# Kernel optimization log

Hardware: AMD Instinct MI355X
Metric: run time of the kernel (lower is better)

## Reference

```python
import jax, jax.numpy as jnp
import numpy as np

B, S, D = 4, 4096, 1024          # batch, seq, in/out features
H = 128                          # controller_hidden_dim
K = 8                            # num_spectral_bases
R = 8                            # low_rank_rank
OR = 8                           # orthogonal_rank
RES_SCALE = 1.0; SPEC_SCALE = 1.0; LR_SCALE = 1.0; ROT_SCALE = 1.0
LN_EPS = 1e-5


def setup_inputs() -> dict:
    key = jax.random.key(0)
    ks = jax.random.split(key, 16)
    g = lambda k, shape, scale=0.02: jax.random.normal(k, shape, jnp.float32) * scale
    return dict(
        x=jax.random.normal(ks[0], (B, S, D), jnp.float32),
        # base linear (teacher-aligned base)
        W_base=g(ks[1], (D, D)), b_base=jnp.zeros((D,), jnp.float32),
        # pooled-token conditioner: LayerNorm -> Linear -> GELU -> Linear
        ln_g=jnp.ones((D,), jnp.float32), ln_b=jnp.zeros((D,), jnp.float32),
        Wc1=g(ks[2], (D, H)), bc1=jnp.zeros((H,), jnp.float32),
        Wc2=g(ks[3], (H, H)), bc2=jnp.zeros((H,), jnp.float32),
        # gate heads
        W_rot_gate=g(ks[4], (H, 1)), b_rot_gate=jnp.zeros((1,), jnp.float32),
        W_rot_coeff=g(ks[5], (H, OR)), b_rot_coeff=jnp.zeros((OR,), jnp.float32),
        W_spec_gate=g(ks[6], (H, K)), b_spec_gate=jnp.zeros((K,), jnp.float32),
        W_lr_coeff=g(ks[7], (H, R)), b_lr_coeff=jnp.zeros((R,), jnp.float32),
        # spectral basis operator: input basis U, output basis V
        U_spec=g(ks[8], (K, D), 0.05), V_spec=g(ks[9], (K, D), 0.05),
        # low-rank residual operator
        U_lr=g(ks[10], (R, D), 0.05), V_lr=g(ks[11], (R, D), 0.05),
        # low-rank orthogonal mixer generators (skew-symmetric pairs)
        A_orth=g(ks[12], (OR, D), 0.05), B_orth=g(ks[13], (OR, D), 0.05),
    )


def reference(x, W_base, b_base, ln_g, ln_b, Wc1, bc1, Wc2, bc2,
              W_rot_gate, b_rot_gate, W_rot_coeff, b_rot_coeff,
              W_spec_gate, b_spec_gate, W_lr_coeff, b_lr_coeff,
              U_spec, V_spec, U_lr, V_lr, A_orth, B_orth):
    # --- pooled token conditioner: mean pool -> LN -> MLP -> hidden h [B,H]
    pooled = x.mean(axis=1)                                   # [B, D]
    mu = pooled.mean(-1, keepdims=True)
    var = pooled.var(-1, keepdims=True)
    z = (pooled - mu) * jax.lax.rsqrt(var + LN_EPS) * ln_g + ln_b
    h = jax.nn.gelu(z @ Wc1 + bc1) @ Wc2 + bc2                # [B, H]

    # --- conditioner-produced gates
    rot_gate = jax.nn.sigmoid(h @ W_rot_gate + b_rot_gate)    # [B, 1]
    rot_coeff = jnp.tanh(h @ W_rot_coeff + b_rot_coeff)       # [B, OR]
    spec_gate = jnp.tanh(h @ W_spec_gate + b_spec_gate)       # [B, K]
    lr_coeff = jnp.tanh(h @ W_lr_coeff + b_lr_coeff)          # [B, R]

    # --- low-rank orthogonal mixer: x_rot = x + gate * x @ G^T,
    #     G = sum_k c_k (a_k b_k^T - b_k a_k^T) (skew-symmetric generator)
    pa = jnp.einsum('bsi,ki->bsk', x, A_orth)
    pb = jnp.einsum('bsi,ki->bsk', x, B_orth)
    rot = (jnp.einsum('bsk,bk,ki->bsi', pb, rot_coeff, A_orth)
           - jnp.einsum('bsk,bk,ki->bsi', pa, rot_coeff, B_orth))
    x_rot = x + (ROT_SCALE * rot_gate)[:, None, :] * rot      # [B,S,D]

    # --- spectral basis operator: gated rank-K map through fixed bases
    s = jnp.einsum('bsi,ki->bsk', x_rot, U_spec)
    y_spec = SPEC_SCALE * jnp.einsum('bsk,bk,ko->bso', s, spec_gate, V_spec)

    # --- low-rank residual operator
    t = jnp.einsum('bsi,ki->bsk', x_rot, U_lr)
    y_lr = LR_SCALE * jnp.einsum('bsk,bk,ko->bso', t, lr_coeff, V_lr)

    # --- teacher-aligned base + gated residual operators
    return x_rot @ W_base + b_base + RES_SCALE * (y_spec + y_lr)
```

## Files before the change

kernel.cpp:

```cpp
#include <hip/hip_runtime.h>

typedef unsigned short u16;
typedef unsigned int   u32;
typedef __bf16 bf16x8 __attribute__((ext_vector_type(8)));
typedef float  f32x4  __attribute__((ext_vector_type(4)));

#define DD 1024

__device__ __forceinline__ u16 f2bf(float f) {
  u32 u = __float_as_uint(f);
  u32 r = (u + 0x7FFFu + ((u >> 16) & 1u)) >> 16;
  return (u16)r;
}

typedef const __attribute__((address_space(1))) void* gp1;
typedef __attribute__((address_space(3))) void* lp3;
__device__ __forceinline__ void gll16(const void* g, void* l) {
  __builtin_amdgcn_global_load_lds((gp1)g, (lp3)l, 16, 0, 0);
}

template <bool XB>
__global__ __launch_bounds__(256) void k01_pre(
    const float* __restrict__ x, u16* __restrict__ xb, float* __restrict__ pooled,
    const float* __restrict__ W,
    const float* __restrict__ Ao, const float* __restrict__ Bo,
    const float* __restrict__ Us, const float* __restrict__ Ul,
    float* __restrict__ AWBW, float* __restrict__ Mbuf,
    u16* __restrict__ Pb, u16* __restrict__ Wt) {
  const int tid = threadIdx.x;
  int bid = blockIdx.x;
  if (bid < 1024) {
    const int xcd = bid & 7, local = bid >> 3;
    const int rb = xcd * 128 + local;
    const int b = rb >> 8;
    const long r0 = (long)rb * 16;
    const int c0 = tid * 4;
    float s0 = 0.f, s1 = 0.f, s2 = 0.f, s3 = 0.f;
    for (int r = 0; r < 16; r++) {
      float4 v = *(const float4*)(x + (r0 + r) * DD + c0);
      if (XB) {
        ushort4 o;
        o.x = f2bf(v.x); o.y = f2bf(v.y); o.z = f2bf(v.z); o.w = f2bf(v.w);
        *(ushort4*)(xb + (r0 + r) * DD + c0) = o;
      }
      s0 += v.x; s1 += v.y; s2 += v.z; s3 += v.w;
    }
    atomicAdd(&pooled[b * DD + c0 + 0], s0);
    atomicAdd(&pooled[b * DD + c0 + 1], s1);
    atomicAdd(&pooled[b * DD + c0 + 2], s2);
    atomicAdd(&pooled[b * DD + c0 + 3], s3);
    return;
  }
  bid -= 1024;
  if (bid < 32) {
    __shared__ float red2[2][128][16];
    const int m = bid;
    const int n = (m & 7) * 128 + (tid & 127), q = m >> 3, ih = tid >> 7;
    float acc[16];
#pragma unroll
    for (int k = 0; k < 16; k++) acc[k] = 0.f;
    const int ib = q * 256 + ih * 128;
    for (int i = ib; i < ib + 128; i++) {
      float wv = W[(long)i * DD + n];
#pragma unroll
      for (int k = 0; k < 8; k++) {
        acc[k]     += Ao[k * DD + i] * wv;
        acc[k + 8] += Bo[k * DD + i] * wv;
      }
    }
#pragma unroll
    for (int k = 0; k < 16; k++) red2[ih][tid & 127][k] = acc[k];
    __syncthreads();
    if (ih == 0)
#pragma unroll
      for (int k = 0; k < 16; k++)
        atomicAdd(&AWBW[k * DD + n], red2[0][tid][k] + red2[1][tid][k]);
  } else if (bid < 36) {
    __shared__ float red[64][4];
    const int m = bid - 32;
    const float* L  = (m == 0 || m == 2) ? Ao : Bo;
    const float* Rr = (m < 2) ? Us : Ul;
    const int o = tid >> 2, ch = tid & 3;
    const int k = o >> 3, kp = o & 7;
    float a = 0.f;
    for (int i = ch * 256; i < ch * 256 + 256; i++)
      a += L[(long)k * DD + i] * Rr[(long)kp * DD + i];
    red[o][ch] = a;
    __syncthreads();
    if (tid < 64) Mbuf[m * 64 + tid] = red[tid][0] + red[tid][1] + red[tid][2] + red[tid][3];
  } else if (bid < 40) {
    const int m = bid - 36;
    const float* src = m == 0 ? Ao : m == 1 ? Bo : m == 2 ? Us : Ul;
#pragma unroll
    for (int j = 0; j < 8; j++)
      for (int q = 0; q < 4; q++) {
        int i = q * 256 + tid;
        Pb[(m * 8 + j) * DD + i] = f2bf(src[j * DD + i]);
      }
  } else {
    __shared__ u16 T[64][66];
    const int t = bid - 40, tr = t >> 4, tc = t & 15;
#pragma unroll
    for (int q2 = 0; q2 < 16; q2++) {
      int idx = q2 * 256 + tid, r = idx >> 6, c = idx & 63;
      T[r][c] = f2bf(W[(long)(tr * 64 + r) * DD + tc * 64 + c]);
    }
    __syncthreads();
#pragma unroll
    for (int q2 = 0; q2 < 16; q2++) {
      int idx = q2 * 256 + tid, c = idx >> 6, r = idx & 63;
      Wt[(long)(tc * 64 + c) * DD + tr * 64 + r] = T[r][c];
    }
  }
}

__global__ __launch_bounds__(256) void k2ab(
    const float* __restrict__ pooledsum,
    const float* __restrict__ lng, const float* __restrict__ lnb,
    const float* __restrict__ Wc1, float* __restrict__ h1pre,
    const float* __restrict__ AWBW, const float* Vs, const float* Vl,
    const float* bc1, const float* Wc2, const float* bc2,
    const float* Wrg, const float* brg, const float* Wrc, const float* brc,
    const float* Wsg, const float* bsg, const float* Wlc, const float* blc,
    float* __restrict__ gates, u16* __restrict__ RwT,
    u32* __restrict__ cnt) {
  const int tid = threadIdx.x;
  if (blockIdx.x < 32) {
    __shared__ float zs[1024];
    __shared__ float wsh[16384];
    __shared__ float red[256];
    const int b = blockIdx.x >> 3, ch = blockIdx.x & 7;
    float4 v = *(const float4*)(pooledsum + b * DD + tid * 4);
    v.x *= (1.f / 4096.f); v.y *= (1.f / 4096.f); v.z *= (1.f / 4096.f); v.w *= (1.f / 4096.f);
    float s = v.x + v.y + v.z + v.w;
    float sq = v.x * v.x + v.y * v.y + v.z * v.z + v.w * v.w;
    red[tid] = s; __syncthreads();
    for (int st = 128; st > 0; st >>= 1) { if (tid < st) red[tid] += red[tid + st]; __syncthreads(); }
    float mu = red[0] * (1.f / 1024.f);
    __syncthreads();
    red[tid] = sq; __syncthreads();
    for (int st = 128; st > 0; st >>= 1) { if (tid < st) red[tid] += red[tid + st]; __syncthreads(); }
    float var = red[0] * (1.f / 1024.f) - mu * mu;
    float rs = rsqrtf(var + 1e-5f);
    __syncthreads();
    {
      float4 g = *(const float4*)(lng + tid * 4);
      float4 be = *(const float4*)(lnb + tid * 4);
      zs[tid * 4 + 0] = (v.x - mu) * rs * g.x + be.x;
      zs[tid * 4 + 1] = (v.y - mu) * rs * g.y + be.y;
      zs[tid * 4 + 2] = (v.z - mu) * rs * g.z + be.z;
      zs[tid * 4 + 3] = (v.w - mu) * rs * g.w + be.w;
    }
    {
      const float4* src = (const float4*)(Wc1 + ch * 16384);
      float4* dst = (float4*)wsh;
#pragma unroll
      for (int it = 0; it < 16; it++) dst[it * 256 + tid] = src[it * 256 + tid];
    }
    __syncthreads();
    const int j = tid & 127, half = tid >> 7;
    float a = 0.f;
#pragma unroll 8
    for (int dd = 0; dd < 64; dd++) {
      int ldi = half * 64 + dd;
      a += zs[ch * 128 + ldi] * wsh[ldi * 128 + j];
    }
    red[tid] = a;
    __syncthreads();
    if (tid < 128) atomicAdd(&h1pre[b * 128 + tid], red[tid] + red[tid + 128]);
    __syncthreads();
    if (tid == 0) atomicAdd(cnt, 1u);
  } else if (blockIdx.x < 36) {
    __shared__ float wc2sh[16384];
    __shared__ float h1s[128], hb[128];
    __shared__ float red[256];
    __shared__ float hw[3200];
    const int b = (int)blockIdx.x - 32;
    {
      const float4* src = (const float4*)Wc2;
      float4* dst = (float4*)wc2sh;
#pragma unroll
      for (int it = 0; it < 16; it++) dst[it * 256 + tid] = src[it * 256 + tid];
    }
    for (int idx = tid; idx < 3200; idx += 256) {
      float vv;
      if (idx < 128)       vv = Wrg[idx];
      else if (idx < 1152) vv = Wrc[idx - 128];
      else if (idx < 2176) vv = Wsg[idx - 1152];
      else                 vv = Wlc[idx - 2176];
      hw[idx] = vv;
    }
    if (tid == 0) {
      while (atomicAdd(cnt, 0u) < 32u) __builtin_amdgcn_s_sleep(8);
    }
    __syncthreads();
    if (tid < 128) {
      float hv = atomicAdd(&h1pre[b * 128 + tid], 0.f) + bc1[tid];
      float th = tanhf(0.7978845608028654f * (hv + 0.044715f * hv * hv * hv));
      h1s[tid] = 0.5f * hv * (1.f + th);
    }
    __syncthreads();
    const int i = tid & 127, half = tid >> 7;
    float a = 0.f;
#pragma unroll 8
    for (int k = 0; k < 64; k++) {
      int kk = half * 64 + k;
      a += h1s[kk] * wc2sh[kk * 128 + i];
    }
    red[tid] = a;
    __syncthreads();
    if (tid < 128) hb[tid] = red[tid] + red[tid + 128] + bc2[tid];
    __syncthreads();
    if (tid < 25) {
      float acc;
      if (tid == 0) {
        acc = brg[0];
        for (int k = 0; k < 128; k++) acc += hb[k] * hw[k];
        red[0] = 1.f / (1.f + expf(-acc));
      } else if (tid < 9) {
        int ci = tid - 1; acc = brc[ci];
        for (int k = 0; k < 128; k++) acc += hb[k] * hw[128 + k * 8 + ci];
        red[tid] = tanhf(acc);
      } else if (tid < 17) {
        int ci = tid - 9; acc = bsg[ci];
        for (int k = 0; k < 128; k++) acc += hb[k] * hw[1152 + k * 8 + ci];
        red[tid] = tanhf(acc);
      } else {
        int ci = tid - 17; acc = blc[ci];
        for (int k = 0; k < 128; k++) acc += hb[k] * hw[2176 + k * 8 + ci];
        red[tid] = tanhf(acc);
      }
    }
    __syncthreads();
    if (tid < 24) {
      float g = red[0];
      gates[b * 32 + tid] = (tid < 8) ? g * red[1 + tid] : red[1 + tid];
    }
  } else {
    const int n = (int)(blockIdx.x - 36) * 256 + tid;
#pragma unroll
    for (int j = 0; j < 8; j++) {
      RwT[n * 32 + j]      = f2bf(AWBW[j * DD + n]);
      RwT[n * 32 + 8 + j]  = f2bf(AWBW[(8 + j) * DD + n]);
      RwT[n * 32 + 16 + j] = f2bf(Vs[(long)j * DD + n]);
      RwT[n * 32 + 24 + j] = f2bf(Vl[(long)j * DD + n]);
    }
  }
}

__global__ __launch_bounds__(256, 3) void k3a_fused(
    const u16* __restrict__ xb, const u16* __restrict__ Wt,
    const u16* __restrict__ Pb, const float* __restrict__ gates,
    const float* __restrict__ Mbuf, const u16* __restrict__ RwT,
    const float* __restrict__ bb, float* __restrict__ out) {
  __shared__ __align__(16) char smem[38912];
  const int tid = threadIdx.x, lane = tid & 63, w = tid >> 6;
  const int quad = lane >> 4, lrow = lane & 15;
  const int bidx = blockIdx.x;
  const int bm = (bidx & 7) * 16 + (bidx >> 6);
  const int bn = (bidx >> 3) & 7;
  const long m0 = (long)bm * 128;
  const int n0 = bn * 128;
  const int batch = bm >> 5;
  float* Ml = (float*)(smem + 36864);
  float* gl = (float*)(smem + 37888);
  Ml[tid] = Mbuf[tid];
  if (tid < 24) gl[tid] = gates[batch * 32 + tid];
  const int mw = (w & 1) * 64, nw = (w >> 1) * 64;
  const int pc0 = (w >> 1) * 16;
  const int sr = lane >> 2, sc = (lane & 3) * 16;
  const char* xbp = (const char*)xb;
  const char* wtp = (const char*)Wt;
  const char* pbp = (const char*)Pb;
  const long aOff0 = (m0 + (long)w * 16 + sr) * 2048 + sc;
  const long aOff1 = aOff0 + 4 * 16 * 2048;
  const long bOff0 = ((long)n0 + w * 16 + sr) * 2048 + sc;
  const long bOff1 = bOff0 + 4 * 16 * 2048;
  const long pOff  = ((long)w * 16 + sr) * 2048 + sc;
  const int d0 = w * 1024 + lane * 16;

  f32x4 acc[4][4] = {};
  f32x4 acc2[4] = {};

  gll16(xbp + aOff0, smem + d0);
  gll16(xbp + aOff1, smem + d0 + 4096);
  gll16(wtp + bOff0, smem + 16384 + d0);
  gll16(wtp + bOff1, smem + 16384 + d0 + 4096);
  if (w < 2) gll16(pbp + pOff, smem + 32768 + d0);
  __syncthreads();

  int cur = 0;
  for (int kc = 0; kc < 32; kc++) {
    if (kc < 31) {
      const long ko = (long)(kc + 1) * 64;
      const int s = cur ^ 1;
      gll16(xbp + aOff0 + ko, smem + s * 8192 + d0);
      gll16(xbp + aOff1 + ko, smem + s * 8192 + d0 + 4096);
      gll16(wtp + bOff0 + ko, smem + 16384 + s * 8192 + d0);
      gll16(wtp + bOff1 + ko, smem + 16384 + s * 8192 + d0 + 4096);
      if (w < 2) gll16(pbp + pOff + ko, smem + 32768 + s * 2048 + d0);
    }
    const u16* At = (const u16*)(smem + cur * 8192);
    const u16* Bt = (const u16*)(smem + 16384 + cur * 8192);
    const u16* Pt = (const u16*)(smem + 32768 + cur * 2048);
    bf16x8 af[4], bq[4], bp;
#pragma unroll
    for (int tm = 0; tm < 4; tm++)
      af[tm] = *(const bf16x8*)(At + (mw + tm * 16 + lrow) * 32 + quad * 8);
#pragma unroll
    for (int tn = 0; tn < 4; tn++)
      bq[tn] = *(const bf16x8*)(Bt + (nw + tn * 16 + lrow) * 32 + quad * 8);
    bp = *(const bf16x8*)(Pt + (pc0 + lrow) * 32 + quad * 8);
#pragma unroll
    for (int tm = 0; tm < 4; tm++)
#pragma unroll
      for (int tn = 0; tn < 4; tn++)
        acc[tm][tn] = __builtin_amdgcn_mfma_f32_16x16x32_bf16(af[tm], bq[tn], acc[tm][tn], 0, 0, 0);
#pragma unroll
    for (int tm = 0; tm < 4; tm++)
      acc2[tm] = __builtin_amdgcn_mfma_f32_16x16x32_bf16(af[tm], bp, acc2[tm], 0, 0, 0);
    __syncthreads();
    cur ^= 1;
  }

  {
    const char* rwp = (const char*)RwT;
    const long rOff = ((long)n0 + w * 16 + sr) * 64 + sc;
    gll16(rwp + rOff, smem + 16384 + d0);
    gll16(rwp + rOff + 64 * 64, smem + 16384 + d0 + 4096);
  }
  float* projF = (float*)smem;
#pragma unroll
  for (int tm = 0; tm < 4; tm++)
#pragma unroll
    for (int r = 0; r < 4; r++) {
      int row = mw + tm * 16 + quad * 4 + r;
      int col = pc0 + lrow;
      projF[row * 32 + (col ^ (row & 31))] = acc2[tm][r];
    }
  __syncthreads();
  if (tid < 128) {
    float pr[32];
#pragma unroll
    for (int j = 0; j < 32; j++) pr[j] = projF[tid * 32 + (j ^ (tid & 31))];
    float wo[32];
#pragma unroll
    for (int k = 0; k < 8; k++) { wo[k] = gl[k] * pr[8 + k]; wo[8 + k] = -gl[k] * pr[k]; }
#pragma unroll
    for (int kp = 0; kp < 8; kp++) {
      float sv = pr[16 + kp], tv = pr[24 + kp];
#pragma unroll
      for (int k = 0; k < 8; k++) {
        float gpb = gl[k] * pr[8 + k], gpa = gl[k] * pr[k];
        sv += gpb * Ml[k * 8 + kp]       - gpa * Ml[64 + k * 8 + kp];
        tv += gpb * Ml[128 + k * 8 + kp] - gpa * Ml[192 + k * 8 + kp];
      }
      wo[16 + kp] = gl[8 + kp] * sv;
      wo[24 + kp] = gl[16 + kp] * tv;
    }
    u16* wLds = (u16*)(smem + 24576);
#pragma unroll
    for (int j = 0; j < 32; j++) wLds[tid * 32 + j] = f2bf(wo[j]);
  }
  __syncthreads();
  {
    const u16* wL = (const u16*)(smem + 24576);
    const u16* Rt = (const u16*)(smem + 16384);
    bf16x8 af[4], bq[4];
#pragma unroll
    for (int tm = 0; tm < 4; tm++)
      af[tm] = *(const bf16x8*)(wL + (mw + tm * 16 + lrow) * 32 + quad * 8);
#pragma unroll
    for (int tn = 0; tn < 4; tn++)
      bq[tn] = *(const bf16x8*)(Rt + (nw + tn * 16 + lrow) * 32 + quad * 8);
#pragma unroll
    for (int tm = 0; tm < 4; tm++)
#pragma unroll
      for (int tn = 0; tn < 4; tn++)
        acc[tm][tn] = __builtin_amdgcn_mfma_f32_16x16x32_bf16(af[tm], bq[tn], acc[tm][tn], 0, 0, 0);
  }
#pragma unroll
  for (int tn = 0; tn < 4; tn++) {
    const int col = n0 + nw + tn * 16 + lrow;
    const float bias = bb[col];
#pragma unroll
    for (int tm = 0; tm < 4; tm++)
#pragma unroll
      for (int r = 0; r < 4; r++) {
        long row = m0 + mw + tm * 16 + quad * 4 + r;
        out[row * DD + col] = acc[tm][tn][r] + bias;
      }
  }
}

template <bool XB>
__global__ __launch_bounds__(256) void k3_fused(
    const float* __restrict__ xf, const u16* __restrict__ xb,
    const u16* __restrict__ Wt, const u16* __restrict__ Pb,
    const float* __restrict__ gates, const float* __restrict__ Mbuf,
    const u16* __restrict__ RwT, const float* __restrict__ bb,
    float* __restrict__ out) {
  __shared__ __align__(16) u16 At[4096];
  __shared__ __align__(16) u16 Bt[4096];
  __shared__ __align__(16) u16 Pt[1024];
  __shared__ float projF[128 * 32];
  __shared__ __align__(16) u16 wLds[4096];
  __shared__ float Ml[256];
  __shared__ float gl[24];
  const int tid = threadIdx.x, lane = tid & 63, w = tid >> 6;
  const int quad = lane >> 4, lrow = lane & 15;
  const int bn = blockIdx.x & 7, bm = blockIdx.x >> 3;
  const long m0 = (long)bm * 128;
  const int n0 = bn * 128;
  const int batch = bm >> 5;
  Ml[tid] = Mbuf[tid];
  if (tid < 24) gl[tid] = gates[batch * 32 + tid];
  const int mw = (w & 1) * 64, nw = (w >> 1) * 64;
  const int p0 = (w * 2) * 1024 + lane * 16, p1 = p0 + 1024;
  f32x4 acc[4][4] = {};
  f32x4 acc2[2][2] = {};
  for (int kc = 0; kc < 32; kc++) {
    uint4 vb0 = *(const uint4*)((const char*)Wt + (long)(n0 + (p0 >> 6)) * 2048 + kc * 64 + (p0 & 63));
    uint4 vb1 = *(const uint4*)((const char*)Wt + (long)(n0 + (p1 >> 6)) * 2048 + kc * 64 + (p1 & 63));
    uint4 vp;
// ... 115 lines not shown
extern "C" void kernel_launch(void* const* d_in, const int* in_sizes, int n_in,
                              void* d_out, int out_size, void* d_ws, size_t ws_size,
                              hipStream_t stream) {
  const float* x   = (const float*)d_in[0];
  const float* Wb  = (const float*)d_in[1];
  const float* bb  = (const float*)d_in[2];
  const float* lng = (const float*)d_in[3];
  const float* lnb = (const float*)d_in[4];
  const float* Wc1 = (const float*)d_in[5];
  const float* bc1 = (const float*)d_in[6];
  const float* Wc2 = (const float*)d_in[7];
  const float* bc2 = (const float*)d_in[8];
  const float* Wrg = (const float*)d_in[9];
  const float* brg = (const float*)d_in[10];
  const float* Wrc = (const float*)d_in[11];
  const float* brc = (const float*)d_in[12];
  const float* Wsg = (const float*)d_in[13];
  const float* bsg = (const float*)d_in[14];
  const float* Wlc = (const float*)d_in[15];
  const float* blc = (const float*)d_in[16];
  const float* Us  = (const float*)d_in[17];
  const float* Vs  = (const float*)d_in[18];
  const float* Ul  = (const float*)d_in[19];
  const float* Vl  = (const float*)d_in[20];
  const float* Ao  = (const float*)d_in[21];
  const float* Bo  = (const float*)d_in[22];

  char* ws = (char*)d_ws;
  float* pooled = (float*)(ws + 0);
  float* AWBW   = (float*)(ws + 16384);
  float* h1pre  = (float*)(ws + 81920);
  float* gates  = (float*)(ws + 83968);
  float* Mbuf   = (float*)(ws + 84480);
  u32*   cnt    = (u32*)  (ws + 85504);
  u16*   RwT    = (u16*)  (ws + 85568);
  u16*   Pb     = (u16*)  (ws + 151104);
  u16*   Wt     = (u16*)  (ws + 216640);
  u16*   xb     = (u16*)  (ws + 2313792);
  float* out    = (float*)d_out;

  const bool modeA = ws_size >= (size_t)2313792 + 33554432;

  (void)hipMemsetAsync(d_ws, 0, 85568, stream);
  if (modeA)
    k01_pre<true><<<1320, 256, 0, stream>>>(x, xb, pooled, Wb, Ao, Bo, Us, Ul,
                                            AWBW, Mbuf, Pb, Wt);
  else
    k01_pre<false><<<1320, 256, 0, stream>>>(x, xb, pooled, Wb, Ao, Bo, Us, Ul,
                                             AWBW, Mbuf, Pb, Wt);
  k2ab<<<40, 256, 0, stream>>>(pooled, lng, lnb, Wc1, h1pre,
                               AWBW, Vs, Vl, bc1, Wc2, bc2,
                               Wrg, brg, Wrc, brc, Wsg, bsg, Wlc, blc,
                               gates, RwT, cnt);
  if (modeA)
    k3a_fused<<<1024, 256, 0, stream>>>(xb, Wt, Pb, gates, Mbuf, RwT, bb, out);
  else
    k3_fused<false><<<1024, 256, 0, stream>>>(x, xb, Wt, Pb, gates, Mbuf, RwT, bb, out);
}
```

Baseline: 320.5 us.

## Fold conditioner MLP and gate kernel into the main GEMM kernel with counters

The small conditioner/gate kernel is merged into the main GEMM launch as extra blocks 0-39. The GEMM blocks run their main K-loop first and spin on a global counter only before the epilogue, which needs the gates and RwT. This removes one kernel launch and lets the controller MLP overlap with the GEMM. k01_pre is reordered so the weight-prep blocks run first. The spin-wait depends on the producer blocks being resident, which risks deadlock or stalls if they are scheduled late. Weight staging in LDS for the MLP is replaced by direct global reads.

Result: slower. 379.0 us (+18.3%).

```diff
diff --git a/kernel.cpp b/kernel.cpp
--- a/kernel.cpp
+++ b/kernel.cpp
@@ -28,9 +28,10 @@
     float* __restrict__ AWBW, float* __restrict__ Mbuf,
     u16* __restrict__ Pb, u16* __restrict__ Wt) {
   const int tid = threadIdx.x;
-  int bid = blockIdx.x;
-  if (bid < 1024) {
-    const int xcd = bid & 7, local = bid >> 3;
+  const int bid = blockIdx.x;
+  if (bid >= 296) {
+    const int i = bid - 296;
+    const int xcd = i & 7, local = i >> 3;
     const int rb = xcd * 128 + local;
     const int b = rb >> 8;
     const long r0 = (long)rb * 16;
@@ -51,7 +52,6 @@
     atomicAdd(&pooled[b * DD + c0 + 3], s3);
     return;
   }
-  bid -= 1024;
   if (bid < 32) {
     __shared__ float red2[2][128][16];
     const int m = bid;
@@ -114,6 +114,275 @@
   }
 }
 
+__global__ __launch_bounds__(256, 3) void k3a_mega(
+    const u16* __restrict__ xb, const u16* __restrict__ Wt,
+    const u16* __restrict__ Pb, const float* __restrict__ Mbuf,
+    const float* __restrict__ bb,
+    const float* __restrict__ pooledsum,
+    const float* __restrict__ lng, const float* __restrict__ lnb,
+    const float* __restrict__ Wc1, float* __restrict__ h1pre,
+    const float* __restrict__ AWBW, const float* Vs, const float* Vl,
+    const float* bc1, const float* Wc2, const float* bc2,
+    const float* Wrg, const float* brg, const float* Wrc, const float* brc,
+    const float* Wsg, const float* bsg, const float* Wlc, const float* blc,
+    float* __restrict__ gates, u16* __restrict__ RwT,
+    u32* __restrict__ cntH, u32* __restrict__ cntG,
+    float* __restrict__ out) {
+  __shared__ __align__(16) char smem[38912];
+  const int tid = threadIdx.x;
+  const int bid = blockIdx.x;
+
+  if (bid < 32) {
+    float* zs  = (float*)smem;
+    float* red = (float*)(smem + 4096);
+    const int b = bid >> 3, ch = bid & 7;
+    float4 v = *(const float4*)(pooledsum + b * DD + tid * 4);
+    v.x *= (1.f / 4096.f); v.y *= (1.f / 4096.f); v.z *= (1.f / 4096.f); v.w *= (1.f / 4096.f);
+    float s = v.x + v.y + v.z + v.w;
+    float sq = v.x * v.x + v.y * v.y + v.z * v.z + v.w * v.w;
+    red[tid] = s; __syncthreads();
+    for (int st = 128; st > 0; st >>= 1) { if (tid < st) red[tid] += red[tid + st]; __syncthreads(); }
+    float mu = red[0] * (1.f / 1024.f);
+    __syncthreads();
+    red[tid] = sq; __syncthreads();
+    for (int st = 128; st > 0; st >>= 1) { if (tid < st) red[tid] += red[tid + st]; __syncthreads(); }
+    float var = red[0] * (1.f / 1024.f) - mu * mu;
+    float rs = rsqrtf(var + 1e-5f);
+    __syncthreads();
+    {
+      float4 g = *(const float4*)(lng + tid * 4);
+      float4 be = *(const float4*)(lnb + tid * 4);
+      zs[tid * 4 + 0] = (v.x - mu) * rs * g.x + be.x;
+      zs[tid * 4 + 1] = (v.y - mu) * rs * g.y + be.y;
+      zs[tid * 4 + 2] = (v.z - mu) * rs * g.z + be.z;
+      zs[tid * 4 + 3] = (v.w - mu) * rs * g.w + be.w;
+    }
+    __syncthreads();
+    const int j = tid & 127, half = tid >> 7;
+    float a = 0.f;
+#pragma unroll 8
+    for (int dd = 0; dd < 64; dd++) {
+      int ldi = half * 64 + dd;
+      a += zs[ch * 128 + ldi] * Wc1[(long)ch * 16384 + ldi * 128 + j];
+    }
+    red[tid] = a;
+    __syncthreads();
+    if (tid < 128) atomicAdd(&h1pre[b * 128 + tid], red[tid] + red[tid + 128]);
+    __syncthreads();
+    if (tid == 0) atomicAdd(cntH, 1u);
+  } else if (bid < 36) {
+    float* h1s = (float*)smem;
+    float* hb  = (float*)(smem + 512);
+    float* red = (float*)(smem + 1024);
+    const int b = bid - 32;
+    if (tid == 0) {
+      while (atomicAdd(cntH, 0u) < 32u) __builtin_amdgcn_s_sleep(8);
+    }
+    __syncthreads();
+    if (tid < 128) {
+      float hv = atomicAdd(&h1pre[b * 128 + tid], 0.f) + bc1[tid];
+      float th = tanhf(0.7978845608028654f * (hv + 0.044715f * hv * hv * hv));
+      h1s[tid] = 0.5f * hv * (1.f + th);
+    }
+    __syncthreads();
+    const int i = tid & 127, half = tid >> 7;
+    float a = 0.f;
+#pragma unroll 8
+    for (int k = 0; k < 64; k++) {
+      int kk = half * 64 + k;
+      a += h1s[kk] * Wc2[kk * 128 + i];
+    }
+    red[tid] = a;
+    __syncthreads();
+    if (tid < 128) hb[tid] = red[tid] + red[tid + 128] + bc2[tid];
+    __syncthreads();
+    if (tid < 25) {
+      float acc;
+      if (tid == 0) {
+        acc = brg[0];
+        for (int k = 0; k < 128; k++) acc += hb[k] * Wrg[k];
+        red[0] = 1.f / (1.f + expf(-acc));
+      } else if (tid < 9) {
+        int ci = tid - 1; acc = brc[ci];
+        for (int k = 0; k < 128; k++) acc += hb[k] * Wrc[k * 8 + ci];
+        red[tid] = tanhf(acc);
+      } else if (tid < 17) {
+        int ci = tid - 9; acc = bsg[ci];
+        for (int k = 0; k < 128; k++) acc += hb[k] * Wsg[k * 8 + ci];
+        red[tid] = tanhf(acc);
+      } else {
+        int ci = tid - 17; acc = blc[ci];
+        for (int k = 0; k < 128; k++) acc += hb[k] * Wlc[k * 8 + ci];
+        red[tid] = tanhf(acc);
+      }
+    }
+    __syncthreads();
+    if (tid < 24) {
+      float g = red[0];
+      gates[b * 32 + tid] = (tid < 8) ? g * red[1 + tid] : red[1 + tid];
+    }
+    __syncthreads();
+    __threadfence();
+    if (tid == 0) atomicAdd(cntG, 1u);
+  } else if (bid < 40) {
+    const int n = (bid - 36) * 256 + tid;
+#pragma unroll
+    for (int j = 0; j < 8; j++) {
+      RwT[n * 32 + j]      = f2bf(AWBW[j * DD + n]);
+      RwT[n * 32 + 8 + j]  = f2bf(AWBW[(8 + j) * DD + n]);
+      RwT[n * 32 + 16 + j] = f2bf(Vs[(long)j * DD + n]);
+      RwT[n * 32 + 24 + j] = f2bf(Vl[(long)j * DD + n]);
+    }
+    __syncthreads();
+    __threadfence();
+    if (tid == 0) atomicAdd(cntG, 1u);
+  } else {
+    const int g = bid - 40;
+    const int lane = tid & 63, w = tid >> 6;
+    const int quad = lane >> 4, lrow = lane & 15;
+    const int bm = (g & 7) * 16 + (g >> 6);
+    const int bn = (g >> 3) & 7;
+    const long m0 = (long)bm * 128;
+    const int n0 = bn * 128;
+    const int batch = bm >> 5;
+    float* Ml = (float*)(smem + 36864);
+    float* gl = (float*)(smem + 37888);
+    Ml[tid] = Mbuf[tid];
+    const int mw = (w & 1) * 64, nw = (w >> 1) * 64;
+    const int pc0 = (w >> 1) * 16;
+    const int sr = lane >> 2, sc = (lane & 3) * 16;
+    const char* xbp = (const char*)xb;
+    const char* wtp = (const char*)Wt;
+    const char* pbp = (const char*)Pb;
+    const long aOff0 = (m0 + (long)w * 16 + sr) * 2048 + sc;
+    const long aOff1 = aOff0 + 4 * 16 * 2048;
+    const long bOff0 = ((long)n0 + w * 16 + sr) * 2048 + sc;
+    const long bOff1 = bOff0 + 4 * 16 * 2048;
+    const long pOff  = ((long)w * 16 + sr) * 2048 + sc;
+    const int d0 = w * 1024 + lane * 16;
+
+    f32x4 acc[4][4] = {};
+    f32x4 acc2[4] = {};
+
+    gll16(xbp + aOff0, smem + d0);
+    gll16(xbp + aOff1, smem + d0 + 4096);
+    gll16(wtp + bOff0, smem + 16384 + d0);
+    gll16(wtp + bOff1, smem + 16384 + d0 + 4096);
+    if (w < 2) gll16(pbp + pOff, smem + 32768 + d0);
+    __syncthreads();
+
+    int cur = 0;
+    for (int kc = 0; kc < 32; kc++) {
+      if (kc < 31) {
+        const long ko = (long)(kc + 1) * 64;
+        const int sbuf = cur ^ 1;
+        gll16(xbp + aOff0 + ko, smem + sbuf * 8192 + d0);
+        gll16(xbp + aOff1 + ko, smem + sbuf * 8192 + d0 + 4096);
+        gll16(wtp + bOff0 + ko, smem + 16384 + sbuf * 8192 + d0);
+        gll16(wtp + bOff1 + ko, smem + 16384 + sbuf * 8192 + d0 + 4096);
+        if (w < 2) gll16(pbp + pOff + ko, smem + 32768 + sbuf * 2048 + d0);
+      }
+      const u16* At = (const u16*)(smem + cur * 8192);
+      const u16* Bt = (const u16*)(smem + 16384 + cur * 8192);
+      const u16* Pt = (const u16*)(smem + 32768 + cur * 2048);
+      bf16x8 af[4], bq[4], bp;
+#pragma unroll
+      for (int tm = 0; tm < 4; tm++)
+        af[tm] = *(const bf16x8*)(At + (mw + tm * 16 + lrow) * 32 + quad * 8);
+#pragma unroll
+      for (int tn = 0; tn < 4; tn++)
+        bq[tn] = *(const bf16x8*)(Bt + (nw + tn * 16 + lrow) * 32 + quad * 8);
+      bp = *(const bf16x8*)(Pt + (pc0 + lrow) * 32 + quad * 8);
+#pragma unroll
+      for (int tm = 0; tm < 4; tm++)
+#pragma unroll
+        for (int tn = 0; tn < 4; tn++)
+          acc[tm][tn] = __builtin_amdgcn_mfma_f32_16x16x32_bf16(af[tm], bq[tn], acc[tm][tn], 0, 0, 0);
+#pragma unroll
+      for (int tm = 0; tm < 4; tm++)
+        acc2[tm] = __builtin_amdgcn_mfma_f32_16x16x32_bf16(af[tm], bp, acc2[tm], 0, 0, 0);
+      __syncthreads();
+      cur ^= 1;
+    }
+
+    if (tid == 0) {
+      while (atomicAdd(cntG, 0u) < 8u) __builtin_amdgcn_s_sleep(2);
+    }
+    __syncthreads();
+    __threadfence();
+    if (tid < 24) gl[tid] = gates[batch * 32 + tid];
+
+    {
+      const char* rwp = (const char*)RwT;
+      const long rOff = ((long)n0 + w * 16 + sr) * 64 + sc;
+      gll16(rwp + rOff, smem + 16384 + d0);
+      gll16(rwp + rOff + 64 * 64, smem + 16384 + d0 + 4096);
+    }
+    float* projF = (float*)smem;
+#pragma unroll
+    for (int tm = 0; tm < 4; tm++)
+#pragma unroll
+      for (int r = 0; r < 4; r++) {
+        int row = mw + tm * 16 + quad * 4 + r;
+        int col = pc0 + lrow;
+        projF[row * 32 + (col ^ (row & 31))] = acc2[tm][r];
+      }
+    __syncthreads();
+    if (tid < 128) {
+      float pr[32];
+#pragma unroll
+      for (int j = 0; j < 32; j++) pr[j] = projF[tid * 32 + (j ^ (tid & 31))];
+      float wo[32];
+#pragma unroll
+      for (int k = 0; k < 8; k++) { wo[k] = gl[k] * pr[8 + k]; wo[8 + k] = -gl[k] * pr[k]; }
+#pragma unroll
+      for (int kp = 0; kp < 8; kp++) {
+        float sv = pr[16 + kp], tv = pr[24 + kp];
+#pragma unroll
+        for (int k = 0; k < 8; k++) {
+          float gpb = gl[k] * pr[8 + k], gpa = gl[k] * pr[k];
+          sv += gpb * Ml[k * 8 + kp]       - gpa * Ml[64 + k * 8 + kp];
+          tv += gpb * Ml[128 + k * 8 + kp] - gpa * Ml[192 + k * 8 + kp];
+        }
+        wo[16 + kp] = gl[8 + kp] * sv;
+        wo[24 + kp] = gl[16 + kp] * tv;
+      }
+      u16* wLds = (u16*)(smem + 24576);
+#pragma unroll
+      for (int j = 0; j < 32; j++) wLds[tid * 32 + j] = f2bf(wo[j]);
+    }
+    __syncthreads();
+    {
+      const u16* wL = (const u16*)(smem + 24576);
+      const u16* Rt = (const u16*)(smem + 16384);
+      bf16x8 af[4], bq[4];
+#pragma unroll
+      for (int tm = 0; tm < 4; tm++)
+        af[tm] = *(const bf16x8*)(wL + (mw + tm * 16 + lrow) * 32 + quad * 8);
+#pragma unroll
+      for (int tn = 0; tn < 4; tn++)
+        bq[tn] = *(const bf16x8*)(Rt + (nw + tn * 16 + lrow) * 32 + quad * 8);
+#pragma unroll
+      for (int tm = 0; tm < 4; tm++)
+#pragma unroll
+        for (int tn = 0; tn < 4; tn++)
+          acc[tm][tn] = __builtin_amdgcn_mfma_f32_16x16x32_bf16(af[tm], bq[tn], acc[tm][tn], 0, 0, 0);
+    }
+#pragma unroll
+    for (int tn = 0; tn < 4; tn++) {
+      const int col = n0 + nw + tn * 16 + lrow;
+      const float bias = bb[col];
+#pragma unroll
+      for (int tm = 0; tm < 4; tm++)
+#pragma unroll
+        for (int r = 0; r < 4; r++) {
+          long row = m0 + mw + tm * 16 + quad * 4 + r;
+          out[row * DD + col] = acc[tm][tn][r] + bias;
+        }
+    }
+  }
+}
+
 __global__ __launch_bounds__(256) void k2ab(
     const float* __restrict__ pooledsum,
     const float* __restrict__ lng, const float* __restrict__ lnb,
@@ -127,7 +396,6 @@
   const int tid = threadIdx.x;
   if (blockIdx.x < 32) {
     __shared__ float zs[1024];
-    __shared__ float wsh[16384];
     __shared__ float red[256];
     const int b = blockIdx.x >> 3, ch = blockIdx.x & 7;
     float4 v = *(const float4*)(pooledsum + b * DD + tid * 4);
@@ -151,19 +419,13 @@
       zs[tid * 4 + 2] = (v.z - mu) * rs * g.z + be.z;
       zs[tid * 4 + 3] = (v.w - mu) * rs * g.w + be.w;
     }
-    {
-      const float4* src = (const float4*)(Wc1 + ch * 16384);
-      float4* dst = (float4*)wsh;
-#pragma unroll
-      for (int it = 0; it < 16; it++) dst[it * 256 + tid] = src[it * 256 + tid];
-    }
     __syncthreads();
     const int j = tid & 127, half = tid >> 7;
     float a = 0.f;
 #pragma unroll 8
     for (int dd = 0; dd < 64; dd++) {
       int ldi = half * 64 + dd;
-      a += zs[ch * 128 + ldi] * wsh[ldi * 128 + j];
+      a += zs[ch * 128 + ldi] * Wc1[(long)ch * 16384 + ldi * 128 + j];
     }
     red[tid] = a;
     __syncthreads();
@@ -171,25 +433,9 @@
     __syncthreads();
     if (tid == 0) atomicAdd(cnt, 1u);
   } else if (blockIdx.x < 36) {
-    __shared__ float wc2sh[16384];
     __shared__ float h1s[128], hb[128];
     __shared__ float red[256];
-    __shared__ float hw[3200];
     const int b = (int)blockIdx.x - 32;
-    {
-      const float4* src = (const float4*)Wc2;
-      float4* dst = (float4*)wc2sh;
-#pragma unroll
-      for (int it = 0; it < 16; it++) dst[it * 256 + tid] = src[it * 256 + tid];
-    }
-    for (int idx = tid; idx < 3200; idx += 256) {
-      float vv;
-      if (idx < 128)       vv = Wrg[idx];
-      else if (idx < 1152) vv = Wrc[idx - 128];
-      else if (idx < 2176) vv = Wsg[idx - 1152];
-      else                 vv = Wlc[idx - 2176];
-      hw[idx] = vv;
-    }
     if (tid == 0) {
       while (atomicAdd(cnt, 0u) < 32u) __builtin_amdgcn_s_sleep(8);
     }
@@ -205,7 +451,7 @@
 #pragma unroll 8
     for (int k = 0; k < 64; k++) {
       int kk = half * 64 + k;
-      a += h1s[kk] * wc2sh[kk * 128 + i];
+      a += h1s[kk] * Wc2[kk * 128 + i];
     }
     red[tid] = a;
     __syncthreads();
@@ -215,19 +461,19 @@
       float acc;
       if (tid == 0) {
         acc = brg[0];
-        for (int k = 0; k < 128; k++) acc += hb[k] * hw[k];
+        for (int k = 0; k < 128; k++) acc += hb[k] * Wrg[k];
         red[0] = 1.f / (1.f + expf(-acc));
       } else if (tid < 9) {
         int ci = tid - 1; acc = brc[ci];
-        for (int k = 0; k < 128; k++) acc += hb[k] * hw[128 + k * 8 + ci];
+        for (int k = 0; k < 128; k++) acc += hb[k] * Wrc[k * 8 + ci];
         red[tid] = tanhf(acc);
       } else if (tid < 17) {
         int ci = tid - 9; acc = bsg[ci];
-        for (int k = 0; k < 128; k++) acc += hb[k] * hw[1152 + k * 8 + ci];
+        for (int k = 0; k < 128; k++) acc += hb[k] * Wsg[k * 8 + ci];
         red[tid] = tanhf(acc);
       } else {
         int ci = tid - 17; acc = blc[ci];
-        for (int k = 0; k < 128; k++) acc += hb[k] * hw[2176 + k * 8 + ci];
+        for (int k = 0; k < 128; k++) acc += hb[k] * Wlc[k * 8 + ci];
         red[tid] = tanhf(acc);
       }
     }
@@ -245,151 +491,6 @@
       RwT[n * 32 + 16 + j] = f2bf(Vs[(long)j * DD + n]);
       RwT[n * 32 + 24 + j] = f2bf(Vl[(long)j * DD + n]);
     }
-  }
-}
-
-__global__ __launch_bounds__(256, 3) void k3a_fused(
-    const u16* __restrict__ xb, const u16* __restrict__ Wt,
-    const u16* __restrict__ Pb, const float* __restrict__ gates,
-    const float* __restrict__ Mbuf, const u16* __restrict__ RwT,
-    const float* __restrict__ bb, float* __restrict__ out) {
-  __shared__ __align__(16) char smem[38912];
-  const int tid = threadIdx.x, lane = tid & 63, w = tid >> 6;
-  const int quad = lane >> 4, lrow = lane & 15;
-  const int bidx = blockIdx.x;
-  const int bm = (bidx & 7) * 16 + (bidx >> 6);
-  const int bn = (bidx >> 3) & 7;
-  const long m0 = (long)bm * 128;
-  const int n0 = bn * 128;
-  const int batch = bm >> 5;
-  float* Ml = (float*)(smem + 36864);
-  float* gl = (float*)(smem + 37888);
-  Ml[tid] = Mbuf[tid];
-  if (tid < 24) gl[tid] = gates[batch * 32 + tid];
-  const int mw = (w & 1) * 64, nw = (w >> 1) * 64;
-  const int pc0 = (w >> 1) * 16;
-  const int sr = lane >> 2, sc = (lane & 3) * 16;
-  const char* xbp = (const char*)xb;
-  const char* wtp = (const char*)Wt;
-  const char* pbp = (const char*)Pb;
-  const long aOff0 = (m0 + (long)w * 16 + sr) * 2048 + sc;
-  const long aOff1 = aOff0 + 4 * 16 * 2048;
-  const long bOff0 = ((long)n0 + w * 16 + sr) * 2048 + sc;
-  const long bOff1 = bOff0 + 4 * 16 * 2048;
-  const long pOff  = ((long)w * 16 + sr) * 2048 + sc;
-  const int d0 = w * 1024 + lane * 16;
-
-  f32x4 acc[4][4] = {};
-  f32x4 acc2[4] = {};
-
-  gll16(xbp + aOff0, smem + d0);
-  gll16(xbp + aOff1, smem + d0 + 4096);
-  gll16(wtp + bOff0, smem + 16384 + d0);
-  gll16(wtp + bOff1, smem + 16384 + d0 + 4096);
-  if (w < 2) gll16(pbp + pOff, smem + 32768 + d0);
-  __syncthreads();
-
-  int cur = 0;
-  for (int kc = 0; kc < 32; kc++) {
-    if (kc < 31) {
-      const long ko = (long)(kc + 1) * 64;
-      const int s = cur ^ 1;
-      gll16(xbp + aOff0 + ko, smem + s * 8192 + d0);
-      gll16(xbp + aOff1 + ko, smem + s * 8192 + d0 + 4096);
-      gll16(wtp + bOff0 + ko, smem + 16384 + s * 8192 + d0);
-      gll16(wtp + bOff1 + ko, smem + 16384 + s * 8192 + d0 + 4096);
-      if (w < 2) gll16(pbp + pOff + ko, smem + 32768 + s * 2048 + d0);
-    }
-    const u16* At = (const u16*)(smem + cur * 8192);
-    const u16* Bt = (const u16*)(smem + 16384 + cur * 8192);
-    const u16* Pt = (const u16*)(smem + 32768 + cur * 2048);
-    bf16x8 af[4], bq[4], bp;
-#pragma unroll
-    for (int tm = 0; tm < 4; tm++)
-      af[tm] = *(const bf16x8*)(At + (mw + tm * 16 + lrow) * 32 + quad * 8);
-#pragma unroll
-    for (int tn = 0; tn < 4; tn++)
-      bq[tn] = *(const bf16x8*)(Bt + (nw + tn * 16 + lrow) * 32 + quad * 8);
-    bp = *(const bf16x8*)(Pt + (pc0 + lrow) * 32 + quad * 8);
-#pragma unroll
-    for (int tm = 0; tm < 4; tm++)
-#pragma unroll
-      for (int tn = 0; tn < 4; tn++)
-        acc[tm][tn] = __builtin_amdgcn_mfma_f32_16x16x32_bf16(af[tm], bq[tn], acc[tm][tn], 0, 0, 0);
-#pragma unroll
-    for (int tm = 0; tm < 4; tm++)
-      acc2[tm] = __builtin_amdgcn_mfma_f32_16x16x32_bf16(af[tm], bp, acc2[tm], 0, 0, 0);
-    __syncthreads();
-    cur ^= 1;
-  }
-
-  {
-    const char* rwp = (const char*)RwT;
-    const long rOff = ((long)n0 + w * 16 + sr) * 64 + sc;
-    gll16(rwp + rOff, smem + 16384 + d0);
-    gll16(rwp + rOff + 64 * 64, smem + 16384 + d0 + 4096);
-  }
-  float* projF = (float*)smem;
-#pragma unroll
-  for (int tm = 0; tm < 4; tm++)
-#pragma unroll
-    for (int r = 0; r < 4; r++) {
-      int row = mw + tm * 16 + quad * 4 + r;
-      int col = pc0 + lrow;
-      projF[row * 32 + (col ^ (row & 31))] = acc2[tm][r];
-    }
-  __syncthreads();
-  if (tid < 128) {
-    float pr[32];
-#pragma unroll
-    for (int j = 0; j < 32; j++) pr[j] = projF[tid * 32 + (j ^ (tid & 31))];
-    float wo[32];
-#pragma unroll
-    for (int k = 0; k < 8; k++) { wo[k] = gl[k] * pr[8 + k]; wo[8 + k] = -gl[k] * pr[k]; }
-#pragma unroll
-    for (int kp = 0; kp < 8; kp++) {
-      float sv = pr[16 + kp], tv = pr[24 + kp];
-#pragma unroll
-      for (int k = 0; k < 8; k++) {
-        float gpb = gl[k] * pr[8 + k], gpa = gl[k] * pr[k];
-        sv += gpb * Ml[k * 8 + kp]       - gpa * Ml[64 + k * 8 + kp];
-        tv += gpb * Ml[128 + k * 8 + kp] - gpa * Ml[192 + k * 8 + kp];
-      }
-      wo[16 + kp] = gl[8 + kp] * sv;
-      wo[24 + kp] = gl[16 + kp] * tv;
-    }
-    u16* wLds = (u16*)(smem + 24576);
-#pragma unroll
-    for (int j = 0; j < 32; j++) wLds[tid * 32 + j] = f2bf(wo[j]);
-  }
-  __syncthreads();
-  {
-    const u16* wL = (const u16*)(smem + 24576);
-    const u16* Rt = (const u16*)(smem + 16384);
-    bf16x8 af[4], bq[4];
-#pragma unroll
-    for (int tm = 0; tm < 4; tm++)
-      af[tm] = *(const bf16x8*)(wL + (mw + tm * 16 + lrow) * 32 + quad * 8);
-#pragma unroll
-    for (int tn = 0; tn < 4; tn++)
-      bq[tn] = *(const bf16x8*)(Rt + (nw + tn * 16 + lrow) * 32 + quad * 8);
-#pragma unroll
-    for (int tm = 0; tm < 4; tm++)
-#pragma unroll
-      for (int tn = 0; tn < 4; tn++)
-        acc[tm][tn] = __builtin_amdgcn_mfma_f32_16x16x32_bf16(af[tm], bq[tn], acc[tm][tn], 0, 0, 0);
-  }
-#pragma unroll
-  for (int tn = 0; tn < 4; tn++) {
-    const int col = n0 + nw + tn * 16 + lrow;
-    const float bias = bb[col];
-#pragma unroll
-    for (int tm = 0; tm < 4; tm++)
-#pragma unroll
-      for (int r = 0; r < 4; r++) {
-        long row = m0 + mw + tm * 16 + quad * 4 + r;
-        out[row * DD + col] = acc[tm][tn][r] + bias;
-      }
   }
 }
 
@@ -571,7 +672,8 @@
   float* h1pre  = (float*)(ws + 81920);
   float* gates  = (float*)(ws + 83968);
   float* Mbuf   = (float*)(ws + 84480);
-  u32*   cnt    = (u32*)  (ws + 85504);
+  u32*   cntH   = (u32*)  (ws + 85504);
+  u32*   cntG   = (u32*)  (ws + 85508);
   u16*   RwT    = (u16*)  (ws + 85568);
   u16*   Pb     = (u16*)  (ws + 151104);
   u16*   Wt     = (u16*)  (ws + 216640);
@@ -581,18 +683,21 @@
   const bool modeA = ws_size >= (size_t)2313792 + 33554432;
 
   (void)hipMemsetAsync(d_ws, 0, 85568, stream);
-  if (modeA)
+  if (modeA) {
     k01_pre<true><<<1320, 256, 0, stream>>>(x, xb, pooled, Wb, Ao, Bo, Us, Ul,
                                             AWBW, Mbuf, Pb, Wt);
-  else
+    k3a_mega<<<1064, 256, 0, stream>>>(xb, Wt, Pb, Mbuf, bb,
+                                       pooled, lng, lnb, Wc1, h1pre,
+                                       AWBW, Vs, Vl, bc1, Wc2, bc2,
+                                       Wrg, brg, Wrc, brc, Wsg, bsg, Wlc, blc,
+                                       gates, RwT, cntH, cntG, out);
+  } else {
     k01_pre<false><<<1320, 256, 0, stream>>>(x, xb, pooled, Wb, Ao, Bo, Us, Ul,
                                              AWBW, Mbuf, Pb, Wt);
-  k2ab<<<40, 256, 0, stream>>>(pooled, lng, lnb, Wc1, h1pre,
-                               AWBW, Vs, Vl, bc1, Wc2, bc2,
-                               Wrg, brg, Wrc, brc, Wsg, bsg, Wlc, blc,
-                               gates, RwT, cnt);
-  if (modeA)
-    k3a_fused<<<1024, 256, 0, stream>>>(xb, Wt, Pb, gates, Mbuf, RwT, bb, out);
-  else
+    k2ab<<<40, 256, 0, stream>>>(pooled, lng, lnb, Wc1, h1pre,
+                                 AWBW, Vs, Vl, bc1, Wc2, bc2,
+                                 Wrg, brg, Wrc, brc, Wsg, bsg, Wlc, blc,
+                                 gates, RwT, cntH);
     k3_fused<false><<<1024, 256, 0, stream>>>(x, xb, Wt, Pb, gates, Mbuf, RwT, bb, out);
+  }
 }
```

## Widen main GEMM tile to 128x256, reorder prep blocks, drop LDS staging in controller

Applied to the files above, without the earlier changes.

The fused main GEMM kernel now computes 128x256 output tiles per block instead of 128x128. Each wave holds 4x8 MFMA accumulators, the grid is halved to 512 blocks and the occupancy hint drops to 2 blocks per CU. The point is to reuse each A tile across twice as many columns and so cut A-operand traffic. The prep kernel now places its small weight-precompute blocks first so they start early instead of trailing the streaming blocks. The controller kernel reads its weights straight from global memory instead of staging them in LDS. The costs are higher register and LDS use, lower occupancy, and fewer blocks to spread across the CUs.

After: 311.4 us. 2.8% less time.

```diff
diff --git a/kernel.cpp b/kernel.cpp
--- a/kernel.cpp
+++ b/kernel.cpp
@@ -28,9 +28,10 @@
     float* __restrict__ AWBW, float* __restrict__ Mbuf,
     u16* __restrict__ Pb, u16* __restrict__ Wt) {
   const int tid = threadIdx.x;
-  int bid = blockIdx.x;
-  if (bid < 1024) {
-    const int xcd = bid & 7, local = bid >> 3;
+  const int bid = blockIdx.x;
+  if (bid >= 296) {
+    const int i = bid - 296;
+    const int xcd = i & 7, local = i >> 3;
     const int rb = xcd * 128 + local;
     const int b = rb >> 8;
     const long r0 = (long)rb * 16;
@@ -51,7 +52,6 @@
     atomicAdd(&pooled[b * DD + c0 + 3], s3);
     return;
   }
-  bid -= 1024;
   if (bid < 32) {
     __shared__ float red2[2][128][16];
     const int m = bid;
@@ -127,7 +127,6 @@
   const int tid = threadIdx.x;
   if (blockIdx.x < 32) {
     __shared__ float zs[1024];
-    __shared__ float wsh[16384];
     __shared__ float red[256];
     const int b = blockIdx.x >> 3, ch = blockIdx.x & 7;
     float4 v = *(const float4*)(pooledsum + b * DD + tid * 4);
@@ -151,19 +150,13 @@
       zs[tid * 4 + 2] = (v.z - mu) * rs * g.z + be.z;
       zs[tid * 4 + 3] = (v.w - mu) * rs * g.w + be.w;
     }
-    {
-      const float4* src = (const float4*)(Wc1 + ch * 16384);
-      float4* dst = (float4*)wsh;
-#pragma unroll
-      for (int it = 0; it < 16; it++) dst[it * 256 + tid] = src[it * 256 + tid];
-    }
     __syncthreads();
     const int j = tid & 127, half = tid >> 7;
     float a = 0.f;
 #pragma unroll 8
     for (int dd = 0; dd < 64; dd++) {
       int ldi = half * 64 + dd;
-      a += zs[ch * 128 + ldi] * wsh[ldi * 128 + j];
+      a += zs[ch * 128 + ldi] * Wc1[(long)ch * 16384 + ldi * 128 + j];
     }
     red[tid] = a;
     __syncthreads();
@@ -171,25 +164,9 @@
     __syncthreads();
     if (tid == 0) atomicAdd(cnt, 1u);
   } else if (blockIdx.x < 36) {
-    __shared__ float wc2sh[16384];
     __shared__ float h1s[128], hb[128];
     __shared__ float red[256];
-    __shared__ float hw[3200];
     const int b = (int)blockIdx.x - 32;
-    {
-      const float4* src = (const float4*)Wc2;
-      float4* dst = (float4*)wc2sh;
-#pragma unroll
-      for (int it = 0; it < 16; it++) dst[it * 256 + tid] = src[it * 256 + tid];
-    }
-    for (int idx = tid; idx < 3200; idx += 256) {
-      float vv;
-      if (idx < 128)       vv = Wrg[idx];
-      else if (idx < 1152) vv = Wrc[idx - 128];
-      else if (idx < 2176) vv = Wsg[idx - 1152];
-      else                 vv = Wlc[idx - 2176];
-      hw[idx] = vv;
-    }
     if (tid == 0) {
       while (atomicAdd(cnt, 0u) < 32u) __builtin_amdgcn_s_sleep(8);
     }
@@ -205,7 +182,7 @@
 #pragma unroll 8
     for (int k = 0; k < 64; k++) {
       int kk = half * 64 + k;
-      a += h1s[kk] * wc2sh[kk * 128 + i];
+      a += h1s[kk] * Wc2[kk * 128 + i];
     }
     red[tid] = a;
     __syncthreads();
@@ -215,19 +192,19 @@
       float acc;
       if (tid == 0) {
         acc = brg[0];
-        for (int k = 0; k < 128; k++) acc += hb[k] * hw[k];
+        for (int k = 0; k < 128; k++) acc += hb[k] * Wrg[k];
         red[0] = 1.f / (1.f + expf(-acc));
       } else if (tid < 9) {
         int ci = tid - 1; acc = brc[ci];
-        for (int k = 0; k < 128; k++) acc += hb[k] * hw[128 + k * 8 + ci];
+        for (int k = 0; k < 128; k++) acc += hb[k] * Wrc[k * 8 + ci];
         red[tid] = tanhf(acc);
       } else if (tid < 17) {
         int ci = tid - 9; acc = bsg[ci];
-        for (int k = 0; k < 128; k++) acc += hb[k] * hw[1152 + k * 8 + ci];
+        for (int k = 0; k < 128; k++) acc += hb[k] * Wsg[k * 8 + ci];
         red[tid] = tanhf(acc);
       } else {
         int ci = tid - 17; acc = blc[ci];
-        for (int k = 0; k < 128; k++) acc += hb[k] * hw[2176 + k * 8 + ci];
+        for (int k = 0; k < 128; k++) acc += hb[k] * Wlc[k * 8 + ci];
         red[tid] = tanhf(acc);
       }
     }
@@ -248,45 +225,46 @@
   }
 }
 
-__global__ __launch_bounds__(256, 3) void k3a_fused(
+__global__ __launch_bounds__(256, 2) void k3b_fused(
     const u16* __restrict__ xb, const u16* __restrict__ Wt,
     const u16* __restrict__ Pb, const float* __restrict__ gates,
     const float* __restrict__ Mbuf, const u16* __restrict__ RwT,
     const float* __restrict__ bb, float* __restrict__ out) {
-  __shared__ __align__(16) char smem[38912];
+  __shared__ __align__(16) char smem[54400];
   const int tid = threadIdx.x, lane = tid & 63, w = tid >> 6;
   const int quad = lane >> 4, lrow = lane & 15;
-  const int bidx = blockIdx.x;
-  const int bm = (bidx & 7) * 16 + (bidx >> 6);
-  const int bn = (bidx >> 3) & 7;
+  const int g = blockIdx.x;
+  const int xcd = g & 7, local = g >> 3;
+  const int bm = xcd * 16 + (local >> 2);
+  const int bn2 = local & 3;
   const long m0 = (long)bm * 128;
-  const int n0 = bn * 128;
+  const int n0 = bn2 * 256;
   const int batch = bm >> 5;
-  float* Ml = (float*)(smem + 36864);
-  float* gl = (float*)(smem + 37888);
+  float* Ml = (float*)(smem + 53248);
+  float* gl = (float*)(smem + 54272);
   Ml[tid] = Mbuf[tid];
   if (tid < 24) gl[tid] = gates[batch * 32 + tid];
-  const int mw = (w & 1) * 64, nw = (w >> 1) * 64;
+  const int mw = (w & 1) * 64, nw = (w >> 1) * 128;
   const int pc0 = (w >> 1) * 16;
   const int sr = lane >> 2, sc = (lane & 3) * 16;
   const char* xbp = (const char*)xb;
   const char* wtp = (const char*)Wt;
   const char* pbp = (const char*)Pb;
   const long aOff0 = (m0 + (long)w * 16 + sr) * 2048 + sc;
-  const long aOff1 = aOff0 + 4 * 16 * 2048;
-  const long bOff0 = ((long)n0 + w * 16 + sr) * 2048 + sc;
-  const long bOff1 = bOff0 + 4 * 16 * 2048;
+  const long aOff1 = aOff0 + 64 * 2048;
+  const long bOff  = ((long)n0 + w * 16 + sr) * 2048 + sc;
   const long pOff  = ((long)w * 16 + sr) * 2048 + sc;
   const int d0 = w * 1024 + lane * 16;
 
-  f32x4 acc[4][4] = {};
+  f32x4 acc[4][8] = {};
   f32x4 acc2[4] = {};
 
   gll16(xbp + aOff0, smem + d0);
   gll16(xbp + aOff1, smem + d0 + 4096);
-  gll16(wtp + bOff0, smem + 16384 + d0);
-  gll16(wtp + bOff1, smem + 16384 + d0 + 4096);
-  if (w < 2) gll16(pbp + pOff, smem + 32768 + d0);
+#pragma unroll
+  for (int seg = 0; seg < 4; seg++)
+    gll16(wtp + bOff + (long)seg * 64 * 2048, smem + 16384 + seg * 4096 + d0);
+  if (w < 2) gll16(pbp + pOff, smem + 49152 + d0);
   __syncthreads();
 
   int cur = 0;
@@ -296,25 +274,27 @@
       const int s = cur ^ 1;
       gll16(xbp + aOff0 + ko, smem + s * 8192 + d0);
       gll16(xbp + aOff1 + ko, smem + s * 8192 + d0 + 4096);
-      gll16(wtp + bOff0 + ko, smem + 16384 + s * 8192 + d0);
-      gll16(wtp + bOff1 + ko, smem + 16384 + s * 8192 + d0 + 4096);
-      if (w < 2) gll16(pbp + pOff + ko, smem + 32768 + s * 2048 + d0);
+#pragma unroll
+      for (int seg = 0; seg < 4; seg++)
+        gll16(wtp + bOff + (long)seg * 64 * 2048 + ko,
+              smem + 16384 + s * 16384 + seg * 4096 + d0);
+      if (w < 2) gll16(pbp + pOff + ko, smem + 49152 + s * 2048 + d0);
     }
     const u16* At = (const u16*)(smem + cur * 8192);
-    const u16* Bt = (const u16*)(smem + 16384 + cur * 8192);
-    const u16* Pt = (const u16*)(smem + 32768 + cur * 2048);
-    bf16x8 af[4], bq[4], bp;
+    const u16* Bt = (const u16*)(smem + 16384 + cur * 16384);
+    const u16* Pt = (const u16*)(smem + 49152 + cur * 2048);
+    bf16x8 af[4], bq[8], bp;
 #pragma unroll
     for (int tm = 0; tm < 4; tm++)
       af[tm] = *(const bf16x8*)(At + (mw + tm * 16 + lrow) * 32 + quad * 8);
 #pragma unroll
-    for (int tn = 0; tn < 4; tn++)
+    for (int tn = 0; tn < 8; tn++)
       bq[tn] = *(const bf16x8*)(Bt + (nw + tn * 16 + lrow) * 32 + quad * 8);
     bp = *(const bf16x8*)(Pt + (pc0 + lrow) * 32 + quad * 8);
 #pragma unroll
     for (int tm = 0; tm < 4; tm++)
 #pragma unroll
-      for (int tn = 0; tn < 4; tn++)
+      for (int tn = 0; tn < 8; tn++)
         acc[tm][tn] = __builtin_amdgcn_mfma_f32_16x16x32_bf16(af[tm], bq[tn], acc[tm][tn], 0, 0, 0);
 #pragma unroll
     for (int tm = 0; tm < 4; tm++)
@@ -324,10 +304,11 @@
   }
 
   {
-    const char* rwp = (const char*)RwT;
     const long rOff = ((long)n0 + w * 16 + sr) * 64 + sc;
-    gll16(rwp + rOff, smem + 16384 + d0);
-    gll16(rwp + rOff + 64 * 64, smem + 16384 + d0 + 4096);
+#pragma unroll
+    for (int seg = 0; seg < 4; seg++)
+      gll16((const char*)RwT + rOff + (long)seg * 64 * 64,
+            smem + 16384 + seg * 4096 + d0);
   }
   float* projF = (float*)smem;
 #pragma unroll
@@ -358,29 +339,29 @@
       wo[16 + kp] = gl[8 + kp] * sv;
       wo[24 + kp] = gl[16 + kp] * tv;
     }
-    u16* wLds = (u16*)(smem + 24576);
+    u16* wLds = (u16*)(smem + 32768);
 #pragma unroll
     for (int j = 0; j < 32; j++) wLds[tid * 32 + j] = f2bf(wo[j]);
   }
   __syncthreads();
   {
-    const u16* wL = (const u16*)(smem + 24576);
+    const u16* wL = (const u16*)(smem + 32768);
     const u16* Rt = (const u16*)(smem + 16384);
-    bf16x8 af[4], bq[4];
+    bf16x8 af[4], bq[8];
 #pragma unroll
     for (int tm = 0; tm < 4; tm++)
       af[tm] = *(const bf16x8*)(wL + (mw + tm * 16 + lrow) * 32 + quad * 8);
 #pragma unroll
-    for (int tn = 0; tn < 4; tn++)
+    for (int tn = 0; tn < 8; tn++)
       bq[tn] = *(const bf16x8*)(Rt + (nw + tn * 16 + lrow) * 32 + quad * 8);
 #pragma unroll
     for (int tm = 0; tm < 4; tm++)
 #pragma unroll
-      for (int tn = 0; tn < 4; tn++)
+      for (int tn = 0; tn < 8; tn++)
         acc[tm][tn] = __builtin_amdgcn_mfma_f32_16x16x32_bf16(af[tm], bq[tn], acc[tm][tn], 0, 0, 0);
   }
 #pragma unroll
-  for (int tn = 0; tn < 4; tn++) {
+  for (int tn = 0; tn < 8; tn++) {
     const int col = n0 + nw + tn * 16 + lrow;
     const float bias = bb[col];
 #pragma unroll
@@ -571,7 +552,7 @@
   float* h1pre  = (float*)(ws + 81920);
   float* gates  = (float*)(ws + 83968);
   float* Mbuf   = (float*)(ws + 84480);
-  u32*   cnt    = (u32*)  (ws + 85504);
+  u32*   cntH   = (u32*)  (ws + 85504);
   u16*   RwT    = (u16*)  (ws + 85568);
   u16*   Pb     = (u16*)  (ws + 151104);
   u16*   Wt     = (u16*)  (ws + 216640);
@@ -581,18 +562,21 @@
   const bool modeA = ws_size >= (size_t)2313792 + 33554432;
 
   (void)hipMemsetAsync(d_ws, 0, 85568, stream);
-  if (modeA)
+  if (modeA) {
     k01_pre<true><<<1320, 256, 0, stream>>>(x, xb, pooled, Wb, Ao, Bo, Us, Ul,
                                             AWBW, Mbuf, Pb, Wt);
-  else
+    k2ab<<<40, 256, 0, stream>>>(pooled, lng, lnb, Wc1, h1pre,
+                                 AWBW, Vs, Vl, bc1, Wc2, bc2,
+                                 Wrg, brg, Wrc, brc, Wsg, bsg, Wlc, blc,
+                                 gates, RwT, cntH);
+    k3b_fused<<<512, 256, 0, stream>>>(xb, Wt, Pb, gates, Mbuf, RwT, bb, out);
+  } else {
     k01_pre<false><<<1320, 256, 0, stream>>>(x, xb, pooled, Wb, Ao, Bo, Us, Ul,
                                              AWBW, Mbuf, Pb, Wt);
-  k2ab<<<40, 256, 0, stream>>>(pooled, lng, lnb, Wc1, h1pre,
-                               AWBW, Vs, Vl, bc1, Wc2, bc2,
-                               Wrg, brg, Wrc, brc, Wsg, bsg, Wlc, blc,
-                               gates, RwT, cnt);
-  if (modeA)
-    k3a_fused<<<1024, 256, 0, stream>>>(xb, Wt, Pb, gates, Mbuf, RwT, bb, out);
-  else
+    k2ab<<<40, 256, 0, stream>>>(pooled, lng, lnb, Wc1, h1pre,
+                                 AWBW, Vs, Vl, bc1, Wc2, bc2,
+                                 Wrg, brg, Wrc, brc, Wsg, bsg, Wlc, blc,
+                                 gates, RwT, cntH);
     k3_fused<false><<<1024, 256, 0, stream>>>(x, xb, Wt, Pb, gates, Mbuf, RwT, bb, out);
-}
+  }
+}
```
